# Optimization experiments

Measured on AMD Instinct MI355X. Metric: run time of the kernel, lower is better.

The kernel has to match this reference:

```python
import jax, jax.numpy as jnp
import numpy as np

N_NODES = 100000
N_EDGES = 400000
N_GRAPHS = 4096
BN_EPS = 1e-5


def _glorot(key, shape):
    fan_in, fan_out = shape
    lim = np.sqrt(6.0 / (fan_in + fan_out))
    return jax.random.uniform(key, shape, jnp.float32, -lim, lim)


def setup_inputs() -> dict:
    key = jax.random.key(0)
    ks = jax.random.split(key, 16)
    x = jax.random.normal(ks[0], (N_NODES, 373), jnp.float32)
    edge_index = jax.random.randint(ks[1], (2, N_EDGES), 0, N_NODES, jnp.int64)
    batch = jnp.sort(jax.random.randint(ks[2], (N_NODES,), 0, N_GRAPHS, jnp.int64))
    params = {
        # GIN layer 1 MLP: 373->256->256
        'W1a': _glorot(ks[3], (373, 256)), 'b1a': jnp.zeros((256,), jnp.float32),
        'W1b': _glorot(ks[4], (256, 256)), 'b1b': jnp.zeros((256,), jnp.float32),
        'g1': jnp.ones((256,), jnp.float32), 'be1': jnp.zeros((256,), jnp.float32),
        # GIN layer 2 MLP: 256->128->128
        'W2a': _glorot(ks[5], (256, 128)), 'b2a': jnp.zeros((128,), jnp.float32),
        'W2b': _glorot(ks[6], (128, 128)), 'b2b': jnp.zeros((128,), jnp.float32),
        'g2': jnp.ones((128,), jnp.float32), 'be2': jnp.zeros((128,), jnp.float32),
        # GIN layer 3 MLP: 128->64->64
        'W3a': _glorot(ks[7], (128, 64)), 'b3a': jnp.zeros((64,), jnp.float32),
        'W3b': _glorot(ks[8], (64, 64)), 'b3b': jnp.zeros((64,), jnp.float32),
        'g3': jnp.ones((64,), jnp.float32), 'be3': jnp.zeros((64,), jnp.float32),
        # head
        'Wf1': _glorot(ks[9], (64, 16)), 'bf1': jnp.zeros((16,), jnp.float32),
        'Wf2': _glorot(ks[10], (16, 1)), 'bf2': jnp.zeros((1,), jnp.float32),
    }
    return {'x': x, 'edge_index': edge_index, 'batch': batch, **params}


def _gin_conv(x, src, dst, Wa, ba, Wb, bb):
    # sum-aggregate neighbor messages (eps = 0 default in GINConv)
    agg = jax.ops.segment_sum(x[src], dst, num_segments=N_NODES)
    h = x + agg
    h = jax.nn.relu(h @ Wa + ba) @ Wb + bb
    return h


def _batchnorm(x, gamma, beta):
    mu = jnp.mean(x, axis=0)
    var = jnp.var(x, axis=0)
    return (x - mu) * jax.lax.rsqrt(var + BN_EPS) * gamma + beta


def reference(x, edge_index, batch,
              W1a, b1a, W1b, b1b, g1, be1,
              W2a, b2a, W2b, b2b, g2, be2,
              W3a, b3a, W3b, b3b, g3, be3,
              Wf1, bf1, Wf2, bf2):
    src, dst = edge_index[0], edge_index[1]
    h = jax.nn.relu(_gin_conv(x, src, dst, W1a, b1a, W1b, b1b))
    h = _batchnorm(h, g1, be1)
    h = jax.nn.relu(_gin_conv(h, src, dst, W2a, b2a, W2b, b2b))
    h = _batchnorm(h, g2, be2)
    h = jax.nn.relu(_gin_conv(h, src, dst, W3a, b3a, W3b, b3b))
    h = _batchnorm(h, g3, be3)
    # global_add_pool: [N, 64] -> [G, 64]
    pooled = jax.ops.segment_sum(h, batch, num_segments=N_GRAPHS)
    out = jax.nn.relu(pooled @ Wf1 + bf1)
    # dropout omitted (eval mode)
    out = jax.nn.relu(out @ Wf2 + bf2)
    return out.reshape(-1)
```

## Files before the change

kernel.cpp:

```cpp
#include <hip/hip_runtime.h>

#define N_NODES 100000
#define N_EDGES 400000
#define N_GRAPHS 4096
#define BN_EPS 1e-5f
#define DEG_CAP 32

typedef unsigned short ushort_t;
typedef short short8 __attribute__((ext_vector_type(8)));
typedef unsigned short ushort4v __attribute__((ext_vector_type(4)));
typedef unsigned short ushort8v __attribute__((ext_vector_type(8)));
typedef float floatx4 __attribute__((ext_vector_type(4)));

__device__ __forceinline__ ushort_t f2b(float f) {
    union { float f; unsigned u; } v; v.f = f;
    unsigned r = v.u + 0x7fffu + ((v.u >> 16) & 1u);
    return (ushort_t)(r >> 16);
}
__device__ __forceinline__ float b2f(ushort_t b) {
    union { unsigned u; float f; } v; v.u = ((unsigned)b) << 16;
    return v.f;
}

__global__ void k_pad_x(const float* __restrict__ x, ushort_t* __restrict__ xb,
                        int* __restrict__ cursor,
                        const float* __restrict__ W1a, ushort_t* __restrict__ BT1) {
    int t = threadIdx.x;
    if (blockIdx.x >= N_NODES) {
        int b = blockIdx.x - N_NODES;
        int n = b / 3, kc = b % 3;
        int k = kc * 128 + t;
        float v = (k < 373) ? W1a[(long)k * 256 + n] : 0.f;
        BT1[(long)n * 384 + k] = f2b(v);
        return;
    }
    int n = blockIdx.x;
    const float* xr = x + (long)n * 373;
    ushort_t* o = xb + (long)n * 384;
    if (t < 93) {
        float v0 = xr[t * 4 + 0], v1 = xr[t * 4 + 1], v2 = xr[t * 4 + 2], v3 = xr[t * 4 + 3];
        ushort4v s = {f2b(v0), f2b(v1), f2b(v2), f2b(v3)};
        *(ushort4v*)(o + t * 4) = s;
    } else if (t == 93) {
        o[372] = f2b(xr[372]);
        o[373] = 0; o[374] = 0; o[375] = 0;
    } else if (t == 94 || t == 95) {
        ushort4v z = {0, 0, 0, 0};
        *(ushort4v*)(o + 376 + (t - 94) * 4) = z;
    } else if (t == 96) {
        cursor[n] = 0;
    }
}

__global__ void k_fill(const int* __restrict__ src, const int* __restrict__ dst,
                       int* __restrict__ cursor, int* __restrict__ elist) {
    int e = blockIdx.x * blockDim.x + threadIdx.x;
    if (e < N_EDGES) {
        int d = dst[e];
        int slot = atomicAdd(&cursor[d], 1);
        if (slot < DEG_CAP) elist[(long)d * DEG_CAP + slot] = src[e];
    }
}

__global__ void k_prep_scaled(const float* __restrict__ W, const float* __restrict__ scsh,
                              ushort_t* __restrict__ BT, float* __restrict__ biasE,
                              int K, int Kp, int Nn) {
    int n = blockIdx.y;
    int k = blockIdx.x * 128 + threadIdx.x;
    if (k < Kp) {
        float v = (k < K) ? W[(long)k * Nn + n] * scsh[k] : 0.f;
        BT[(long)n * Kp + k] = f2b(v);
    }
    if (blockIdx.x == 0) {
        __shared__ float red[2];
        float s = 0.f;
        for (int kk = threadIdx.x; kk < K; kk += 128) s += scsh[K + kk] * W[(long)kk * Nn + n];
#pragma unroll
        for (int off = 32; off >= 1; off >>= 1) s += __shfl_xor(s, off);
        if ((threadIdx.x & 63) == 0) red[threadIdx.x >> 6] = s;
        __syncthreads();
        if (threadIdx.x == 0) biasE[n] = red[0] + red[1];
    }
}

template<int KP, int TN, bool STATS>
__global__ __launch_bounds__(256) void k_gemm(const ushort_t* __restrict__ A,
                                              const ushort_t* __restrict__ BT,
                                              const float* __restrict__ bias,
                                              ushort_t* __restrict__ C,
                                              float* __restrict__ partials,
                                              int M, int Nn, int relu) {
    __shared__ __align__(16) ushort_t As[2][128 * 32];
    __shared__ __align__(16) ushort_t Bs[2][TN * 32];
    float* swred = (float*)As;
    const int tid = threadIdx.x;
    const int wave = tid >> 6, lane = tid & 63;
    const int ln = lane & 15, kg = lane >> 4;
    const long rowBase = (long)blockIdx.y * 128;
    const int colBase = blockIdx.x * TN;

    constexpr int RT = (TN == 128) ? 4 : 2;
    const int rowOff = (TN == 128) ? ((wave >> 1) * 64) : (wave * 32);
    const int colOff = (TN == 128) ? ((wave & 1) * 64) : 0;

    const ushort_t* aSrc[2];
#pragma unroll
    for (int i = 0; i < 2; i++) {
        long r = rowBase + i * 64 + (tid >> 2);
        if (r >= M) r = M - 1;
        aSrc[i] = A + r * KP + (tid & 3) * 8;
    }
    const ushort_t* bSrc[TN / 64];
#pragma unroll
    for (int i = 0; i < TN / 64; i++) {
        long cc = colBase + i * 64 + (tid >> 2);
        bSrc[i] = BT + cc * KP + (tid & 3) * 8;
    }

    auto stage = [&](int b, int k0) {
#pragma unroll
        for (int i = 0; i < 2; i++)
            __builtin_amdgcn_global_load_lds(
                (const __attribute__((address_space(1))) void*)(aSrc[i] + k0),
                (__attribute__((address_space(3))) void*)(As[b] + wave * 512 + i * 2048), 16, 0, 0);
#pragma unroll
        for (int i = 0; i < TN / 64; i++)
            __builtin_amdgcn_global_load_lds(
                (const __attribute__((address_space(1))) void*)(bSrc[i] + k0),
                (__attribute__((address_space(3))) void*)(Bs[b] + wave * 512 + i * 2048), 16, 0, 0);
    };

    floatx4 acc[RT][4];
#pragma unroll
    for (int i = 0; i < RT; i++)
#pragma unroll
        for (int j = 0; j < 4; j++) acc[i][j] = (floatx4){0.f, 0.f, 0.f, 0.f};

    stage(0, 0);
    int cur = 0;
    for (int k0 = 0; k0 < KP; k0 += 32) {
        __syncthreads();
        if (k0 + 32 < KP) stage(cur ^ 1, k0 + 32);

        short8 afr[RT], bfr[4];
#pragma unroll
        for (int rt = 0; rt < RT; rt++)
            afr[rt] = *(const short8*)&As[cur][(rowOff + rt * 16 + ln) * 32 + kg * 8];
#pragma unroll
        for (int tn = 0; tn < 4; tn++)
            bfr[tn] = *(const short8*)&Bs[cur][(colOff + tn * 16 + ln) * 32 + kg * 8];
#pragma unroll
        for (int rt = 0; rt < RT; rt++)
#pragma unroll
            for (int tn = 0; tn < 4; tn++)
                acc[rt][tn] = __builtin_amdgcn_mfma_f32_16x16x32_bf16(afr[rt], bfr[tn], acc[rt][tn], 0, 0, 0);
        cur ^= 1;
    }

    if constexpr (STATS) {
        __syncthreads();
        for (int i = tid; i < 4 * 2 * TN; i += 256) swred[i] = 0.f;
        __syncthreads();
    }

    float sums[4] = {0.f, 0.f, 0.f, 0.f};
    float sqs[4]  = {0.f, 0.f, 0.f, 0.f};
#pragma unroll
    for (int rt = 0; rt < RT; rt++) {
#pragma unroll
        for (int tn = 0; tn < 4; tn++) {
            int gc = colBase + colOff + tn * 16 + ln;
            float bv = bias ? bias[gc] : 0.f;
#pragma unroll
            for (int r = 0; r < 4; r++) {
                long gr = rowBase + rowOff + rt * 16 + kg * 4 + r;
                if (gr < M) {
                    float v = acc[rt][tn][r] + bv;
                    if (relu) v = fmaxf(v, 0.f);
                    ushort_t sb = f2b(v);
                    C[gr * Nn + gc] = sb;
                    if (STATS) {
                        float vb = b2f(sb);
                        sums[tn] += vb;
                        sqs[tn] += vb * vb;
                    }
                }
            }
        }
    }
    if constexpr (STATS) {
#pragma unroll
        for (int tn = 0; tn < 4; tn++) {
            float s = sums[tn], q = sqs[tn];
            s += __shfl_xor(s, 16); q += __shfl_xor(q, 16);
            s += __shfl_xor(s, 32); q += __shfl_xor(q, 32);
            if (kg == 0) {
                int c = colOff + tn * 16 + ln;
                swred[wave * 2 * TN + c] = s;
                swred[wave * 2 * TN + TN + c] = q;
            }
        }
        __syncthreads();
        const int by = blockIdx.y;
        const int gyd = gridDim.y;
        for (int c = tid; c < TN; c += 256) {
            float ssum = 0.f, ssq = 0.f;
#pragma unroll
            for (int w = 0; w < 4; w++) {
                ssum += swred[w * 2 * TN + c];
                ssq  += swred[w * 2 * TN + TN + c];
            }
            long gc = colBase + c;
            partials[gc * gyd + by] = ssum;
            partials[((long)Nn + gc) * gyd + by] = ssq;
        }
    }
}

template<int KP, int TN>
__global__ __launch_bounds__(256, 4) void k_gemm_agg(const ushort_t* __restrict__ y,
                                                  const int* __restrict__ cursor,
                                                  const int* __restrict__ elist,
                                                  const float* __restrict__ badd,
                                                  const ushort_t* __restrict__ BT,
                                                  const float* __restrict__ bias,
                                                  ushort_t* __restrict__ C,
                                                  float* __restrict__ partials,
                                                  int M, int Nn) {
    __shared__ __align__(16) ushort_t Af[128 * KP];
    __shared__ __align__(16) ushort_t Bs[TN * 32];
    float* swred = (float*)Af;
    const int tid = threadIdx.x;
    const int wave = tid >> 6, lane = tid & 63;
    const int ln = lane & 15, kg = lane >> 4;
    const long rowBase = (long)blockIdx.y * 128;
    constexpr int CPR = KP / 8;
    constexpr int TPR = CPR;
    constexpr int RPS = 256 / TPR;

    {
        const int lr = tid / TPR;
        const int ck = tid % TPR;
        const int c0 = ck * 8;
        float bd[8];
#pragma unroll
        for (int j = 0; j < 8; j++) bd[j] = badd[c0 + j];
        for (int s = 0; s < 128; s += RPS) {
            int r = s + lr;
            long gr = rowBase + r; if (gr >= M) gr = M - 1;
            int cnt = cursor[gr]; if (cnt > DEG_CAP) cnt = DEG_CAP;
            const int* el = elist + gr * DEG_CAP;
            int4 e0 = *(const int4*)el;
            int4 e1 = *(const int4*)(el + 4);
            int ids[8] = {e0.x, e0.y, e0.z, e0.w, e1.x, e1.y, e1.z, e1.w};
            ushort8v sv = *(const ushort8v*)(y + gr * KP + c0);
            ushort8v rr[8];
#pragma unroll
            for (int i = 0; i < 8; i++)
                if (i < cnt) rr[i] = *(const ushort8v*)(y + (long)ids[i] * KP + c0);
            float av[8];
#pragma unroll
            for (int j = 0; j < 8; j++) av[j] = b2f(sv[j]);
#pragma unroll
            for (int i = 0; i < 8; i++)
                if (i < cnt) {
#pragma unroll
                    for (int j = 0; j < 8; j++) av[j] += b2f(rr[i][j]);
                }
            for (int i = 8; i < cnt; i++) {
                ushort8v u = *(const ushort8v*)(y + (long)el[i] * KP + c0);
#pragma unroll
                for (int j = 0; j < 8; j++) av[j] += b2f(u[j]);
            }
            ushort8v ov;
#pragma unroll
            for (int j = 0; j < 8; j++) ov[j] = f2b(fmaxf(av[j] + bd[j], 0.f));
            int cks = ck ^ (r & (CPR - 1));
            *(ushort8v*)&Af[r * KP + cks * 8] = ov;
        }
    }

    constexpr int RT = (TN == 128) ? 4 : 2;
    const int rowOff = (TN == 128) ? ((wave >> 1) * 64) : (wave * 32);
    const int colOff = (TN == 128) ? ((wave & 1) * 64) : 0;
    const ushort_t* bSrc[TN / 64];
#pragma unroll
    for (int i = 0; i < TN / 64; i++) {
        long cc = i * 64 + (tid >> 2);
        bSrc[i] = BT + cc * KP + (tid & 3) * 8;
    }
    ushort_t* bDst = Bs + wave * 512;

    floatx4 acc[RT][4];
#pragma unroll
    for (int i = 0; i < RT; i++)
#pragma unroll
        for (int j = 0; j < 4; j++) acc[i][j] = (floatx4){0.f, 0.f, 0.f, 0.f};

    for (int k0 = 0; k0 < KP; k0 += 32) {
        __syncthreads();
#pragma unroll
        for (int i = 0; i < TN / 64; i++)
            __builtin_amdgcn_global_load_lds(
                (const __attribute__((address_space(1))) void*)(bSrc[i] + k0),
                (__attribute__((address_space(3))) void*)(bDst + i * 2048), 16, 0, 0);
        __syncthreads();

        short8 afr[RT], bfr[4];
#pragma unroll
        for (int rt = 0; rt < RT; rt++) {
            int row = rowOff + rt * 16 + ln;
            int cks = ((k0 >> 3) + kg) ^ (row & (CPR - 1));
            afr[rt] = *(const short8*)&Af[row * KP + cks * 8];
        }
#pragma unroll
        for (int tn = 0; tn < 4; tn++)
            bfr[tn] = *(const short8*)&Bs[(colOff + tn * 16 + ln) * 32 + kg * 8];
#pragma unroll
        for (int rt = 0; rt < RT; rt++)
#pragma unroll
            for (int tn = 0; tn < 4; tn++)
                acc[rt][tn] = __builtin_amdgcn_mfma_f32_16x16x32_bf16(afr[rt], bfr[tn], acc[rt][tn], 0, 0, 0);
    }

    __syncthreads();
    for (int i = tid; i < 4 * 2 * TN; i += 256) swred[i] = 0.f;
    __syncthreads();

    float sums[4] = {0.f, 0.f, 0.f, 0.f};
    float sqs[4]  = {0.f, 0.f, 0.f, 0.f};
#pragma unroll
    for (int rt = 0; rt < RT; rt++) {
#pragma unroll
        for (int tn = 0; tn < 4; tn++) {
            int gc = colOff + tn * 16 + ln;
            float bv = bias[gc];
#pragma unroll
            for (int r = 0; r < 4; r++) {
                long gr = rowBase + rowOff + rt * 16 + kg * 4 + r;
                if (gr < M) {
                    float v = fmaxf(acc[rt][tn][r] + bv, 0.f);
                    ushort_t sb = f2b(v);
                    C[gr * Nn + gc] = sb;
                    float vb = b2f(sb);
                    sums[tn] += vb;
                    sqs[tn] += vb * vb;
                }
            }
        }
    }
#pragma unroll
    for (int tn = 0; tn < 4; tn++) {
        float s = sums[tn], q = sqs[tn];
        s += __shfl_xor(s, 16); q += __shfl_xor(q, 16);
        s += __shfl_xor(s, 32); q += __shfl_xor(q, 32);
        if (kg == 0) {
            int c = colOff + tn * 16 + ln;
            swred[wave * 2 * TN + c] = s;
            swred[wave * 2 * TN + TN + c] = q;
        }
    }
    __syncthreads();
    const int by = blockIdx.y;
    const int gyd = gridDim.y;
    for (int c = tid; c < TN; c += 256) {
        float ssum = 0.f, ssq = 0.f;
#pragma unroll
        for (int w = 0; w < 4; w++) {
            ssum += swred[w * 2 * TN + c];
            ssq  += swred[w * 2 * TN + TN + c];
        }
        partials[(long)c * gyd + by] = ssum;
        partials[((long)Nn + c) * gyd + by] = ssq;
    }
}

template<int D>
__global__ void k_aggregate(const ushort_t* __restrict__ y, const int* __restrict__ cursor,
                            const int* __restrict__ elist, const float* __restrict__ badd,
                            ushort_t* __restrict__ out, int nblk,
                            const float* __restrict__ Wn, ushort_t* __restrict__ BTn,
                            int KWn, int NWn) {
    int t = threadIdx.x;
    if ((int)blockIdx.x >= nblk) {
        int b = blockIdx.x - nblk;
        BTn[(long)b * KWn + t] = f2b(Wn[(long)t * NWn + b]);
        return;
    }
    const int CG = D / 4;
    const int NPB = 256 / CG;
    int n = blockIdx.x * NPB + t / CG;
    int c = (t % CG) * 4;
    if (n >= N_NODES) return;
    int cnt = cursor[n];
    if (cnt > DEG_CAP) cnt = DEG_CAP;
    const int* el = elist + (long)n * DEG_CAP;
    int4 e0 = *(const int4*)el;
    int4 e1 = *(const int4*)(el + 4);
    int ids[8] = {e0.x, e0.y, e0.z, e0.w, e1.x, e1.y, e1.z, e1.w};
    ushort4v sv = *(const ushort4v*)(y + (long)n * D + c);
    ushort4v rr[8];
#pragma unroll
    for (int i = 0; i < 8; i++)
        if (i < cnt) rr[i] = *(const ushort4v*)(y + (long)ids[i] * D + c);
    float t0 = b2f(sv.x), t1 = b2f(sv.y), t2 = b2f(sv.z), t3 = b2f(sv.w);
#pragma unroll
    for (int i = 0; i < 8; i++)
        if (i < cnt) {
            t0 += b2f(rr[i].x); t1 += b2f(rr[i].y); t2 += b2f(rr[i].z); t3 += b2f(rr[i].w);
        }
    for (int i = 8; i < cnt; i++) {
        ushort4v u = *(const ushort4v*)(y + (long)el[i] * D + c);
        t0 += b2f(u.x); t1 += b2f(u.y); t2 += b2f(u.z); t3 += b2f(u.w);
    }
    t0 = fmaxf(t0 + badd[c + 0], 0.f);
    t1 = fmaxf(t1 + badd[c + 1], 0.f);
    t2 = fmaxf(t2 + badd[c + 2], 0.f);
    t3 = fmaxf(t3 + badd[c + 3], 0.f);
    ushort4v o = {f2b(t0), f2b(t1), f2b(t2), f2b(t3)};
    *(ushort4v*)(out + (long)n * D + c) = o;
}

__global__ void k_bn(const float* __restrict__ partials, int gy,
                     const float* __restrict__ gamma, const float* __restrict__ beta,
                     float* __restrict__ scsh, int K,
                     const float* __restrict__ Wn, ushort_t* __restrict__ BTn,
                     int KWn, int NWn) {
    int b = blockIdx.x;
    int t = threadIdx.x;
    if (b >= K) {
        int p = b - K;
        int nk = KWn >> 6;
        int n = p / nk, kc = p - n * nk;
        int k = kc * 64 + t;
        BTn[(long)n * KWn + k] = f2b(Wn[(long)k * NWn + n]);
        return;
    }
    const float* ps = partials + (long)b * gy;
    const float* pq = partials + (long)(K + b) * gy;
    float s = 0.f, q = 0.f;
    for (int i = t; i < gy; i += 64) { s += ps[i]; q += pq[i]; }
#pragma unroll
    for (int off = 32; off >= 1; off >>= 1) { s += __shfl_xor(s, off); q += __shfl_xor(q, off); }
    if (t == 0) {
        float invN = 1.0f / (float)N_NODES;
        float mu = s * invN;
        float var = fmaxf(q * invN - mu * mu, 0.f);
        float sc = rsqrtf(var + BN_EPS) * gamma[b];
        scsh[b] = sc;
        scsh[K + b] = beta[b] - mu * sc;
    }
}

__global__ void k_poolhead(const ushort_t* __restrict__ h, const int* __restrict__ batch,
                           const float* __restrict__ scsh,
                           const float* __restrict__ Wf1, const float* __restrict__ bf1,
                           const float* __restrict__ Wf2, const float* __restrict__ bf2,
                           float* __restrict__ out) {
    __shared__ float pl[64];
    __shared__ float hid[16];
    int g = blockIdx.x;
    int c = threadIdx.x;
    int lo = 0, hi = N_NODES;
    while (lo < hi) { int mid = (lo + hi) >> 1; if (batch[mid] < g) lo = mid + 1; else hi = mid; }
    int start = lo;
    hi = N_NODES;
    while (lo < hi) { int mid = (lo + hi) >> 1; if (batch[mid] < g + 1) lo = mid + 1; else hi = mid; }
    int end = lo;
    float s = 0.f;
    for (int r = start; r < end; r++) s += b2f(h[(long)r * 64 + c]);
    pl[c] = s * scsh[c] + scsh[64 + c] * (float)(end - start);
    __syncthreads();
    if (c < 16) {
        float sh = bf1[c];
        for (int j = 0; j < 64; j++) sh += pl[j] * Wf1[j * 16 + c];
        hid[c] = fmaxf(sh, 0.f);
    }
    __syncthreads();
    if (c == 0) {
        float o = bf2[0];
#pragma unroll
        for (int k = 0; k < 16; k++) o += hid[k] * Wf2[k];
        out[g] = fmaxf(o, 0.f);
    }
}

extern "C" void kernel_launch(void* const* d_in, const int* in_sizes, int n_in,
                              void* d_out, int out_size, void* d_ws, size_t ws_size,
                              hipStream_t stream) {
    const float* x    = (const float*)d_in[0];
    const int*  ei    = (const int*)d_in[1];
    const int*  batch = (const int*)d_in[2];
    const float* W1a = (const float*)d_in[3];
    const float* b1a = (const float*)d_in[4];
    const float* W1b = (const float*)d_in[5];
    const float* b1b = (const float*)d_in[6];
    const float* g1  = (const float*)d_in[7];
    const float* be1 = (const float*)d_in[8];
    const float* W2a = (const float*)d_in[9];
    const float* b2a = (const float*)d_in[10];
    const float* W2b = (const float*)d_in[11];
    const float* b2b = (const float*)d_in[12];
    const float* g2  = (const float*)d_in[13];
    const float* be2 = (const float*)d_in[14];
    const float* W3a = (const float*)d_in[15];
    const float* b3a = (const float*)d_in[16];
    const float* W3b = (const float*)d_in[17];
    const float* b3b = (const float*)d_in[18];
    const float* g3  = (const float*)d_in[19];
    const float* be3 = (const float*)d_in[20];
    const float* Wf1 = (const float*)d_in[21];
    const float* bf1 = (const float*)d_in[22];
    const float* Wf2 = (const float*)d_in[23];
    const float* bf2 = (const float*)d_in[24];

    const int N = N_NODES, E = N_EDGES;
    const int* src = ei;
    const int* dst = ei + E;
    const int gy = (N + 127) / 128;

    char* wp = (char*)d_ws;
    auto carve = [&](size_t bytes) {
        char* p = wp;
        wp += (bytes + 255) & ~(size_t)255;
        return (void*)p;
    };
    ushort_t* xb     = (ushort_t*)carve((size_t)N * 384 * 2);
    ushort_t* bufA   = (ushort_t*)carve((size_t)N * 256 * 2);
    ushort_t* bufB   = (ushort_t*)carve((size_t)N * 256 * 2);
    int*      elist  = (int*)carve((size_t)N * DEG_CAP * 4);
    int*      cursor = (int*)carve((size_t)N * 4);
    ushort_t* BT1    = (ushort_t*)carve((size_t)256 * 384 * 2);
    ushort_t* BT2    = (ushort_t*)carve((size_t)256 * 384 * 2);
    float*    scsh   = (float*)carve(512 * 4);
    float*    biasE  = (float*)carve(256 * 4);
    float*    partials = (float*)carve((size_t)2 * 256 * gy * 4);

    dim3 blk(256);

    k_pad_x<<<N + 768, 128, 0, stream>>>(x, xb, cursor, W1a, BT1);
    k_fill<<<(E + 255) / 256, blk, 0, stream>>>(src, dst, cursor, elist);

    k_gemm<384, 128, false><<<dim3(2, gy), blk, 0, stream>>>(xb, BT1, nullptr, bufA, nullptr, N, 256, 0);
    k_aggregate<256><<<25000 + 256, blk, 0, stream>>>(bufA, cursor, elist, b1a, bufB, 25000, W1b, BT2, 256, 256);
    k_gemm<256, 128, true><<<dim3(2, gy), blk, 0, stream>>>(bufB, BT2, b1b, bufA, partials, N, 256, 1);
    k_bn<<<256 + 256, 64, 0, stream>>>(partials, gy, g1, be1, scsh, 256, W2b, BT2, 128, 128);

    k_prep_scaled<<<dim3(2, 128), 128, 0, stream>>>(W2a, scsh, BT1, biasE, 256, 256, 128);
    k_gemm<256, 128, false><<<dim3(1, gy), blk, 0, stream>>>(bufA, BT1, biasE, bufB, nullptr, N, 128, 0);
    k_gemm_agg<128, 128><<<dim3(1, gy), blk, 0, stream>>>(bufB, cursor, elist, b2a, BT2, b2b, bufA, partials, N, 128);
    k_bn<<<128 + 64, 64, 0, stream>>>(partials, gy, g2, be2, scsh, 128, W3b, BT2, 64, 64);

    k_prep_scaled<<<dim3(1, 64), 128, 0, stream>>>(W3a, scsh, BT1, biasE, 128, 128, 64);
    k_gemm<128, 64, false><<<dim3(1, gy), blk, 0, stream>>>(bufA, BT1, biasE, bufB, nullptr, N, 64, 0);
    k_gemm_agg<64, 64><<<dim3(1, gy), blk, 0, stream>>>(bufB, cursor, elist, b3a, BT2, b3b, bufA, partials, N, 64);
    k_bn<<<64, 64, 0, stream>>>(partials, gy, g3, be3, scsh, 64, nullptr, nullptr, 64, 64);

    k_poolhead<<<N_GRAPHS, 64, 0, stream>>>(bufA, batch, scsh, Wf1, bf1, Wf2, bf2, (float*)d_out);
}
```

Baseline: 614.3 us.

## Fuse layers 2-3, batchnorm and pooling head into one cooperative persistent kernel

Replaces the separate GEMM, gemm_agg, batchnorm, weight-prep and pool-head launches for layers 2 and 3 with a single cooperative kernel. Its phases are separated by grid-wide syncs and it iterates over row tiles persistently. The layer-3 weight transposes are folded into the first BN launch, and the head now handles one graph per wave using shuffle-based reductions. This is meant to remove per-launch overhead and tail effects between the many small kernels. The cost is grid.sync barriers and a grid capped at 1024 blocks, which may cut parallelism in the gather-heavy phases.

```diff
diff --git a/kernel.cpp b/kernel.cpp
--- a/kernel.cpp
+++ b/kernel.cpp
@@ -1,10 +1,14 @@
 #include <hip/hip_runtime.h>
+#include <hip/hip_cooperative_groups.h>
+
+namespace cg = cooperative_groups;
 
 #define N_NODES 100000
 #define N_EDGES 400000
 #define N_GRAPHS 4096
 #define BN_EPS 1e-5f
 #define DEG_CAP 32
+#define GY 782
 
 typedef unsigned short ushort_t;
 typedef short short8 __attribute__((ext_vector_type(8)));
@@ -217,164 +221,6 @@
     }
 }
 
-template<int KP, int TN>
-__global__ __launch_bounds__(256, 4) void k_gemm_agg(const ushort_t* __restrict__ y,
-                                                  const int* __restrict__ cursor,
-                                                  const int* __restrict__ elist,
-                                                  const float* __restrict__ badd,
-                                                  const ushort_t* __restrict__ BT,
-                                                  const float* __restrict__ bias,
-                                                  ushort_t* __restrict__ C,
-                                                  float* __restrict__ partials,
-                                                  int M, int Nn) {
-    __shared__ __align__(16) ushort_t Af[128 * KP];
-    __shared__ __align__(16) ushort_t Bs[TN * 32];
-    float* swred = (float*)Af;
-    const int tid = threadIdx.x;
-    const int wave = tid >> 6, lane = tid & 63;
-    const int ln = lane & 15, kg = lane >> 4;
-    const long rowBase = (long)blockIdx.y * 128;
-    constexpr int CPR = KP / 8;
-    constexpr int TPR = CPR;
-    constexpr int RPS = 256 / TPR;
-
-    {
-        const int lr = tid / TPR;
-        const int ck = tid % TPR;
-        const int c0 = ck * 8;
-        float bd[8];
-#pragma unroll
-        for (int j = 0; j < 8; j++) bd[j] = badd[c0 + j];
-        for (int s = 0; s < 128; s += RPS) {
-            int r = s + lr;
-            long gr = rowBase + r; if (gr >= M) gr = M - 1;
-            int cnt = cursor[gr]; if (cnt > DEG_CAP) cnt = DEG_CAP;
-            const int* el = elist + gr * DEG_CAP;
-            int4 e0 = *(const int4*)el;
-            int4 e1 = *(const int4*)(el + 4);
-            int ids[8] = {e0.x, e0.y, e0.z, e0.w, e1.x, e1.y, e1.z, e1.w};
-            ushort8v sv = *(const ushort8v*)(y + gr * KP + c0);
-            ushort8v rr[8];
-#pragma unroll
-            for (int i = 0; i < 8; i++)
-                if (i < cnt) rr[i] = *(const ushort8v*)(y + (long)ids[i] * KP + c0);
-            float av[8];
-#pragma unroll
-            for (int j = 0; j < 8; j++) av[j] = b2f(sv[j]);
-#pragma unroll
-            for (int i = 0; i < 8; i++)
-                if (i < cnt) {
-#pragma unroll
-                    for (int j = 0; j < 8; j++) av[j] += b2f(rr[i][j]);
-                }
-            for (int i = 8; i < cnt; i++) {
-                ushort8v u = *(const ushort8v*)(y + (long)el[i] * KP + c0);
-#pragma unroll
-                for (int j = 0; j < 8; j++) av[j] += b2f(u[j]);
-            }
-            ushort8v ov;
-#pragma unroll
-            for (int j = 0; j < 8; j++) ov[j] = f2b(fmaxf(av[j] + bd[j], 0.f));
-            int cks = ck ^ (r & (CPR - 1));
-            *(ushort8v*)&Af[r * KP + cks * 8] = ov;
-        }
-    }
-
-    constexpr int RT = (TN == 128) ? 4 : 2;
-    const int rowOff = (TN == 128) ? ((wave >> 1) * 64) : (wave * 32);
-    const int colOff = (TN == 128) ? ((wave & 1) * 64) : 0;
-    const ushort_t* bSrc[TN / 64];
-#pragma unroll
-    for (int i = 0; i < TN / 64; i++) {
-        long cc = i * 64 + (tid >> 2);
-        bSrc[i] = BT + cc * KP + (tid & 3) * 8;
-    }
-    ushort_t* bDst = Bs + wave * 512;
-
-    floatx4 acc[RT][4];
-#pragma unroll
-    for (int i = 0; i < RT; i++)
-#pragma unroll
-        for (int j = 0; j < 4; j++) acc[i][j] = (floatx4){0.f, 0.f, 0.f, 0.f};
-
-    for (int k0 = 0; k0 < KP; k0 += 32) {
-        __syncthreads();
-#pragma unroll
-        for (int i = 0; i < TN / 64; i++)
-            __builtin_amdgcn_global_load_lds(
-                (const __attribute__((address_space(1))) void*)(bSrc[i] + k0),
-                (__attribute__((address_space(3))) void*)(bDst + i * 2048), 16, 0, 0);
-        __syncthreads();
-
-        short8 afr[RT], bfr[4];
-#pragma unroll
-        for (int rt = 0; rt < RT; rt++) {
-            int row = rowOff + rt * 16 + ln;
-            int cks = ((k0 >> 3) + kg) ^ (row & (CPR - 1));
-            afr[rt] = *(const short8*)&Af[row * KP + cks * 8];
-        }
-#pragma unroll
-        for (int tn = 0; tn < 4; tn++)
-            bfr[tn] = *(const short8*)&Bs[(colOff + tn * 16 + ln) * 32 + kg * 8];
-#pragma unroll
-        for (int rt = 0; rt < RT; rt++)
-#pragma unroll
-            for (int tn = 0; tn < 4; tn++)
-                acc[rt][tn] = __builtin_amdgcn_mfma_f32_16x16x32_bf16(afr[rt], bfr[tn], acc[rt][tn], 0, 0, 0);
-    }
-
-    __syncthreads();
-    for (int i = tid; i < 4 * 2 * TN; i += 256) swred[i] = 0.f;
-    __syncthreads();
-
-    float sums[4] = {0.f, 0.f, 0.f, 0.f};
-    float sqs[4]  = {0.f, 0.f, 0.f, 0.f};
-#pragma unroll
-    for (int rt = 0; rt < RT; rt++) {
-#pragma unroll
-        for (int tn = 0; tn < 4; tn++) {
-            int gc = colOff + tn * 16 + ln;
-            float bv = bias[gc];
-#pragma unroll
-            for (int r = 0; r < 4; r++) {
-                long gr = rowBase + rowOff + rt * 16 + kg * 4 + r;
-                if (gr < M) {
-                    float v = fmaxf(acc[rt][tn][r] + bv, 0.f);
-                    ushort_t sb = f2b(v);
-                    C[gr * Nn + gc] = sb;
-                    float vb = b2f(sb);
-                    sums[tn] += vb;
-                    sqs[tn] += vb * vb;
-                }
-            }
-        }
-    }
-#pragma unroll
-    for (int tn = 0; tn < 4; tn++) {
-        float s = sums[tn], q = sqs[tn];
-        s += __shfl_xor(s, 16); q += __shfl_xor(q, 16);
-        s += __shfl_xor(s, 32); q += __shfl_xor(q, 32);
-        if (kg == 0) {
-            int c = colOff + tn * 16 + ln;
-            swred[wave * 2 * TN + c] = s;
-            swred[wave * 2 * TN + TN + c] = q;
-        }
-    }
-    __syncthreads();
-    const int by = blockIdx.y;
-    const int gyd = gridDim.y;
-    for (int c = tid; c < TN; c += 256) {
-        float ssum = 0.f, ssq = 0.f;
-#pragma unroll
-        for (int w = 0; w < 4; w++) {
-            ssum += swred[w * 2 * TN + c];
-            ssq  += swred[w * 2 * TN + TN + c];
-        }
-        partials[(long)c * gyd + by] = ssum;
-        partials[((long)Nn + c) * gyd + by] = ssq;
-    }
-}
-
 template<int D>
 __global__ void k_aggregate(const ushort_t* __restrict__ y, const int* __restrict__ cursor,
                             const int* __restrict__ elist, const float* __restrict__ badd,
@@ -425,15 +271,26 @@
                      const float* __restrict__ gamma, const float* __restrict__ beta,
                      float* __restrict__ scsh, int K,
                      const float* __restrict__ Wn, ushort_t* __restrict__ BTn,
-                     int KWn, int NWn) {
+                     int KWn, int NWn,
+                     const float* __restrict__ Wn2, ushort_t* __restrict__ BTn2,
+                     int KWn2, int NWn2) {
     int b = blockIdx.x;
     int t = threadIdx.x;
     if (b >= K) {
         int p = b - K;
         int nk = KWn >> 6;
-        int n = p / nk, kc = p - n * nk;
-        int k = kc * 64 + t;
-        BTn[(long)n * KWn + k] = f2b(Wn[(long)k * NWn + n]);
+        int tot1 = NWn * nk;
+        if (p < tot1) {
+            int n = p / nk, kc = p - n * nk;
+            int k = kc * 64 + t;
+            BTn[(long)n * KWn + k] = f2b(Wn[(long)k * NWn + n]);
+        } else {
+            p -= tot1;
+            int nk2 = KWn2 >> 6;
+            int n = p / nk2, kc = p - n * nk2;
+            int k = kc * 64 + t;
+            BTn2[(long)n * KWn2 + k] = f2b(Wn2[(long)k * NWn2 + n]);
+        }
         return;
     }
     const float* ps = partials + (long)b * gy;
@@ -452,36 +309,352 @@
     }
 }
 
-__global__ void k_poolhead(const ushort_t* __restrict__ h, const int* __restrict__ batch,
-                           const float* __restrict__ scsh,
-                           const float* __restrict__ Wf1, const float* __restrict__ bf1,
-                           const float* __restrict__ Wf2, const float* __restrict__ bf2,
-                           float* __restrict__ out) {
-    __shared__ float pl[64];
-    __shared__ float hid[16];
-    int g = blockIdx.x;
-    int c = threadIdx.x;
-    int lo = 0, hi = N_NODES;
-    while (lo < hi) { int mid = (lo + hi) >> 1; if (batch[mid] < g) lo = mid + 1; else hi = mid; }
-    int start = lo;
-    hi = N_NODES;
-    while (lo < hi) { int mid = (lo + hi) >> 1; if (batch[mid] < g + 1) lo = mid + 1; else hi = mid; }
-    int end = lo;
-    float s = 0.f;
-    for (int r = start; r < end; r++) s += b2f(h[(long)r * 64 + c]);
-    pl[c] = s * scsh[c] + scsh[64 + c] * (float)(end - start);
+
+template<int KP, int TN>
+__device__ void gemm_tile(char* smem, const ushort_t* __restrict__ A,
+                          const ushort_t* __restrict__ BT, const float* __restrict__ bias,
+                          ushort_t* __restrict__ C, int M, int Nn, int by) {
+    ushort_t* As = (ushort_t*)smem;
+    ushort_t* Bs = (ushort_t*)(smem + 128 * 32 * 2);
+    const int tid = threadIdx.x;
+    const int wave = tid >> 6, lane = tid & 63;
+    const int ln = lane & 15, kg = lane >> 4;
+    const long rowBase = (long)by * 128;
+
+    constexpr int RT = (TN == 128) ? 4 : 2;
+    const int rowOff = (TN == 128) ? ((wave >> 1) * 64) : (wave * 32);
+    const int colOff = (TN == 128) ? ((wave & 1) * 64) : 0;
+
+    const ushort_t* aSrc[2];
+#pragma unroll
+    for (int i = 0; i < 2; i++) {
+        long r = rowBase + i * 64 + (tid >> 2);
+        if (r >= M) r = M - 1;
+        aSrc[i] = A + r * KP + (tid & 3) * 8;
+    }
+    const ushort_t* bSrc[TN / 64];
+#pragma unroll
+    for (int i = 0; i < TN / 64; i++) {
+        long cc = i * 64 + (tid >> 2);
+        bSrc[i] = BT + cc * KP + (tid & 3) * 8;
+    }
+    ushort_t* aDst = As + wave * 512;
+    ushort_t* bDst = Bs + wave * 512;
+
+    floatx4 acc[RT][4];
+#pragma unroll
+    for (int i = 0; i < RT; i++)
+#pragma unroll
+        for (int j = 0; j < 4; j++) acc[i][j] = (floatx4){0.f, 0.f, 0.f, 0.f};
+
+    for (int k0 = 0; k0 < KP; k0 += 32) {
+        __syncthreads();
+#pragma unroll
+        for (int i = 0; i < 2; i++)
+            __builtin_amdgcn_global_load_lds(
+                (const __attribute__((address_space(1))) void*)(aSrc[i] + k0),
+                (__attribute__((address_space(3))) void*)(aDst + i * 2048), 16, 0, 0);
+#pragma unroll
+        for (int i = 0; i < TN / 64; i++)
+            __builtin_amdgcn_global_load_lds(
+                (const __attribute__((address_space(1))) void*)(bSrc[i] + k0),
+                (__attribute__((address_space(3))) void*)(bDst + i * 2048), 16, 0, 0);
+        __syncthreads();
+
+        short8 afr[RT], bfr[4];
+#pragma unroll
+        for (int rt = 0; rt < RT; rt++)
+            afr[rt] = *(const short8*)&As[(rowOff + rt * 16 + ln) * 32 + kg * 8];
+#pragma unroll
+        for (int tn = 0; tn < 4; tn++)
+            bfr[tn] = *(const short8*)&Bs[(colOff + tn * 16 + ln) * 32 + kg * 8];
+#pragma unroll
+        for (int rt = 0; rt < RT; rt++)
+#pragma unroll
+            for (int tn = 0; tn < 4; tn++)
+                acc[rt][tn] = __builtin_amdgcn_mfma_f32_16x16x32_bf16(afr[rt], bfr[tn], acc[rt][tn], 0, 0, 0);
+    }
     __syncthreads();
-    if (c < 16) {
-        float sh = bf1[c];
-        for (int j = 0; j < 64; j++) sh += pl[j] * Wf1[j * 16 + c];
-        hid[c] = fmaxf(sh, 0.f);
-    }
+
+#pragma unroll
+    for (int rt = 0; rt < RT; rt++) {
+#pragma unroll
+        for (int tn = 0; tn < 4; tn++) {
+            int gc = colOff + tn * 16 + ln;
+            float bv = bias[gc];
+#pragma unroll
+            for (int r = 0; r < 4; r++) {
+                long gr = rowBase + rowOff + rt * 16 + kg * 4 + r;
+                if (gr < M) C[gr * Nn + gc] = f2b(acc[rt][tn][r] + bv);
+            }
+        }
+    }
+}
+
+template<int KP, int TN>
+__device__ void gemm_agg_tile(char* smem, const ushort_t* __restrict__ y,
+                              const int* __restrict__ cursor, const int* __restrict__ elist,
+                              const float* __restrict__ badd, const ushort_t* __restrict__ BT,
+                              const float* __restrict__ bias, ushort_t* __restrict__ C,
+                              float* __restrict__ partials, int M, int Nn, int by, int gyd) {
+    ushort_t* Af = (ushort_t*)smem;
+    ushort_t* Bs = (ushort_t*)(smem + 128 * KP * 2);
+    float* swred = (float*)smem;
+    const int tid = threadIdx.x;
+    const int wave = tid >> 6, lane = tid & 63;
+    const int ln = lane & 15, kg = lane >> 4;
+    const long rowBase = (long)by * 128;
+    constexpr int CPR = KP / 8;
+    constexpr int TPR = CPR;
+    constexpr int RPS = 256 / TPR;
+
     __syncthreads();
-    if (c == 0) {
-        float o = bf2[0];
-#pragma unroll
-        for (int k = 0; k < 16; k++) o += hid[k] * Wf2[k];
-        out[g] = fmaxf(o, 0.f);
+
+    {
+        const int lr = tid / TPR;
+        const int ck = tid % TPR;
+        const int c0 = ck * 8;
+        float bd[8];
+#pragma unroll
+        for (int j = 0; j < 8; j++) bd[j] = badd[c0 + j];
+        for (int s = 0; s < 128; s += RPS) {
+            int r = s + lr;
+            long gr = rowBase + r; if (gr >= M) gr = M - 1;
+            int cnt = cursor[gr]; if (cnt > DEG_CAP) cnt = DEG_CAP;
+            const int* el = elist + gr * DEG_CAP;
+            int4 e0 = *(const int4*)el;
+            int4 e1 = *(const int4*)(el + 4);
+            int ids[8] = {e0.x, e0.y, e0.z, e0.w, e1.x, e1.y, e1.z, e1.w};
+            ushort8v sv = *(const ushort8v*)(y + gr * KP + c0);
+            ushort8v rr[8];
+#pragma unroll
+            for (int i = 0; i < 8; i++)
+                if (i < cnt) rr[i] = *(const ushort8v*)(y + (long)ids[i] * KP + c0);
+            float av[8];
+#pragma unroll
+            for (int j = 0; j < 8; j++) av[j] = b2f(sv[j]);
+#pragma unroll
+            for (int i = 0; i < 8; i++)
+                if (i < cnt) {
+#pragma unroll
+                    for (int j = 0; j < 8; j++) av[j] += b2f(rr[i][j]);
+                }
+            for (int i = 8; i < cnt; i++) {
+                ushort8v u = *(const ushort8v*)(y + (long)el[i] * KP + c0);
+#pragma unroll
+                for (int j = 0; j < 8; j++) av[j] += b2f(u[j]);
+            }
+            ushort8v ov;
+#pragma unroll
+            for (int j = 0; j < 8; j++) ov[j] = f2b(fmaxf(av[j] + bd[j], 0.f));
+            int cks = ck ^ (r & (CPR - 1));
+            *(ushort8v*)&Af[r * KP + cks * 8] = ov;
+        }
+    }
+
+    constexpr int RT = (TN == 128) ? 4 : 2;
+    const int rowOff = (TN == 128) ? ((wave >> 1) * 64) : (wave * 32);
+    const int colOff = (TN == 128) ? ((wave & 1) * 64) : 0;
+    const ushort_t* bSrc[TN / 64];
+#pragma unroll
+    for (int i = 0; i < TN / 64; i++) {
+        long cc = i * 64 + (tid >> 2);
+        bSrc[i] = BT + cc * KP + (tid & 3) * 8;
+    }
+    ushort_t* bDst = Bs + wave * 512;
+
+    floatx4 acc[RT][4];
+#pragma unroll
+    for (int i = 0; i < RT; i++)
+#pragma unroll
+        for (int j = 0; j < 4; j++) acc[i][j] = (floatx4){0.f, 0.f, 0.f, 0.f};
+
+    for (int k0 = 0; k0 < KP; k0 += 32) {
+        __syncthreads();
+#pragma unroll
+        for (int i = 0; i < TN / 64; i++)
+            __builtin_amdgcn_global_load_lds(
+                (const __attribute__((address_space(1))) void*)(bSrc[i] + k0),
+                (__attribute__((address_space(3))) void*)(bDst + i * 2048), 16, 0, 0);
+        __syncthreads();
+
+        short8 afr[RT], bfr[4];
+#pragma unroll
+        for (int rt = 0; rt < RT; rt++) {
+            int row = rowOff + rt * 16 + ln;
+            int cks = ((k0 >> 3) + kg) ^ (row & (CPR - 1));
+            afr[rt] = *(const short8*)&Af[row * KP + cks * 8];
+        }
+#pragma unroll
+        for (int tn = 0; tn < 4; tn++)
+            bfr[tn] = *(const short8*)&Bs[(colOff + tn * 16 + ln) * 32 + kg * 8];
+#pragma unroll
+        for (int rt = 0; rt < RT; rt++)
+#pragma unroll
+            for (int tn = 0; tn < 4; tn++)
+                acc[rt][tn] = __builtin_amdgcn_mfma_f32_16x16x32_bf16(afr[rt], bfr[tn], acc[rt][tn], 0, 0, 0);
+    }
+
+    __syncthreads();
+    for (int i = tid; i < 4 * 2 * TN; i += 256) swred[i] = 0.f;
+    __syncthreads();
+
+    float sums[4] = {0.f, 0.f, 0.f, 0.f};
+    float sqs[4]  = {0.f, 0.f, 0.f, 0.f};
+#pragma unroll
+    for (int rt = 0; rt < RT; rt++) {
+#pragma unroll
+        for (int tn = 0; tn < 4; tn++) {
+            int gc = colOff + tn * 16 + ln;
+            float bv = bias[gc];
+#pragma unroll
+            for (int r = 0; r < 4; r++) {
+                long gr = rowBase + rowOff + rt * 16 + kg * 4 + r;
+                if (gr < M) {
+                    float v = fmaxf(acc[rt][tn][r] + bv, 0.f);
+                    ushort_t sb = f2b(v);
+                    C[gr * Nn + gc] = sb;
+                    float vb = b2f(sb);
+                    sums[tn] += vb;
+                    sqs[tn] += vb * vb;
+                }
+            }
+        }
+    }
+#pragma unroll
+    for (int tn = 0; tn < 4; tn++) {
+        float s = sums[tn], q = sqs[tn];
+        s += __shfl_xor(s, 16); q += __shfl_xor(q, 16);
+        s += __shfl_xor(s, 32); q += __shfl_xor(q, 32);
+        if (kg == 0) {
+            int c = colOff + tn * 16 + ln;
+            swred[wave * 2 * TN + c] = s;
+            swred[wave * 2 * TN + TN + c] = q;
+        }
+    }
+    __syncthreads();
+    for (int c = tid; c < TN; c += 256) {
+        float ssum = 0.f, ssq = 0.f;
+#pragma unroll
+        for (int w = 0; w < 4; w++) {
+            ssum += swred[w * 2 * TN + c];
+            ssq  += swred[w * 2 * TN + TN + c];
+        }
+        partials[(long)c * gyd + by] = ssum;
+        partials[((long)Nn + c) * gyd + by] = ssq;
+    }
+    __syncthreads();
+}
+
+__device__ void bn_phase(char* smem, const float* __restrict__ partials, int gy,
+                         const float* __restrict__ gamma, const float* __restrict__ beta,
+                         float* __restrict__ scsh, int K) {
+    float* red = (float*)smem;
+    int wave = threadIdx.x >> 6, lane = threadIdx.x & 63;
+    for (int b = blockIdx.x; b < K; b += gridDim.x) {
+        const float* ps = partials + (long)b * gy;
+        const float* pq = partials + (long)(K + b) * gy;
+        float s = 0.f, q = 0.f;
+        for (int i = threadIdx.x; i < gy; i += 256) { s += ps[i]; q += pq[i]; }
+#pragma unroll
+        for (int off = 32; off >= 1; off >>= 1) { s += __shfl_xor(s, off); q += __shfl_xor(q, off); }
+        if (lane == 0) { red[wave] = s; red[4 + wave] = q; }
+        __syncthreads();
+        if (threadIdx.x == 0) {
+            s = red[0] + red[1] + red[2] + red[3];
+            q = red[4] + red[5] + red[6] + red[7];
+            float invN = 1.0f / (float)N_NODES;
+            float mu = s * invN;
+            float var = fmaxf(q * invN - mu * mu, 0.f);
+            float sc = rsqrtf(var + BN_EPS) * gamma[b];
+            scsh[b] = sc;
+            scsh[K + b] = beta[b] - mu * sc;
+        }
+        __syncthreads();
+    }
+}
+
+__global__ __launch_bounds__(256, 4) void k_tail(
+    ushort_t* bufA, ushort_t* bufB, const int* cursor, const int* elist,
+    const ushort_t* BT2a, const float* biasE2a, const float* b2a,
+    const ushort_t* BT2b, const float* b2b,
+    float* partials, float* scsh,
+    const float* g2, const float* be2,
+    const float* W3a, ushort_t* BT3a, float* biasE3, const float* b3a,
+    const ushort_t* BT3b, const float* b3b,
+    const float* g3, const float* be3,
+    const int* batch, const float* Wf1, const float* bf1,
+    const float* Wf2, const float* bf2, float* outp) {
+    cg::grid_group grid = cg::this_grid();
+    __shared__ __align__(16) char smem[40960];
+
+    for (int by = blockIdx.x; by < GY; by += gridDim.x)
+        gemm_tile<256, 128>(smem, bufA, BT2a, biasE2a, bufB, N_NODES, 128, by);
+    grid.sync();
+
+    for (int by = blockIdx.x; by < GY; by += gridDim.x)
+        gemm_agg_tile<128, 128>(smem, bufB, cursor, elist, b2a, BT2b, b2b, bufA, partials, N_NODES, 128, by, GY);
+    grid.sync();
+
+    bn_phase(smem, partials, GY, g2, be2, scsh, 128);
+    grid.sync();
+
+    {
+        float* red = (float*)smem;
+        int wave = threadIdx.x >> 6, lane = threadIdx.x & 63;
+        for (int n = blockIdx.x; n < 64; n += gridDim.x) {
+            int t = threadIdx.x;
+            float p = 0.f;
+            if (t < 128) {
+                float w = W3a[(long)t * 64 + n];
+                BT3a[n * 128 + t] = f2b(w * scsh[t]);
+                p = scsh[128 + t] * w;
+            }
+#pragma unroll
+            for (int off = 32; off >= 1; off >>= 1) p += __shfl_xor(p, off);
+            if (lane == 0) red[wave] = p;
+            __syncthreads();
+            if (t == 0) biasE3[n] = red[0] + red[1] + red[2] + red[3];
+            __syncthreads();
+        }
+    }
+    grid.sync();
+
+    for (int by = blockIdx.x; by < GY; by += gridDim.x)
+        gemm_tile<128, 64>(smem, bufA, BT3a, biasE3, bufB, N_NODES, 64, by);
+    grid.sync();
+
+    for (int by = blockIdx.x; by < GY; by += gridDim.x)
+        gemm_agg_tile<64, 64>(smem, bufB, cursor, elist, b3a, BT3b, b3b, bufA, partials, N_NODES, 64, by, GY);
+    grid.sync();
+
+    bn_phase(smem, partials, GY, g3, be3, scsh + 256, 64);
+    grid.sync();
+
+    {
+        const float* sc3 = scsh + 256;
+        int wave = threadIdx.x >> 6, lane = threadIdx.x & 63;
+        for (int g = blockIdx.x * 4 + wave; g < N_GRAPHS; g += gridDim.x * 4) {
+            int lo = 0, hi = N_NODES;
+            while (lo < hi) { int mid = (lo + hi) >> 1; if (batch[mid] < g) lo = mid + 1; else hi = mid; }
+            int start = lo;
+            hi = N_NODES;
+            while (lo < hi) { int mid = (lo + hi) >> 1; if (batch[mid] < g + 1) lo = mid + 1; else hi = mid; }
+            int end = lo;
+            float pl = 0.f;
+            for (int r = start; r < end; r++) pl += b2f(bufA[(long)r * 64 + lane]);
+            pl = pl * sc3[lane] + sc3[64 + lane] * (float)(end - start);
+            float hid = 0.f;
+            for (int j = 0; j < 64; j++) {
+                float v = __shfl(pl, j);
+                if (lane < 16) hid += v * Wf1[j * 16 + lane];
+            }
+            float p = 0.f;
+            if (lane < 16) p = fmaxf(hid + bf1[lane], 0.f) * Wf2[lane];
+            p += __shfl_xor(p, 8); p += __shfl_xor(p, 4);
+            p += __shfl_xor(p, 2); p += __shfl_xor(p, 1);
+            if (lane == 0) outp[g] = fmaxf(p + bf2[0], 0.f);
+        }
     }
 }
 
@@ -517,7 +690,7 @@
     const int N = N_NODES, E = N_EDGES;
     const int* src = ei;
     const int* dst = ei + E;
-    const int gy = (N + 127) / 128;
+    const int gy = GY;
 
     char* wp = (char*)d_ws;
     auto carve = [&](size_t bytes) {
@@ -532,9 +705,13 @@
     int*      cursor = (int*)carve((size_t)N * 4);
     ushort_t* BT1    = (ushort_t*)carve((size_t)256 * 384 * 2);
     ushort_t* BT2    = (ushort_t*)carve((size_t)256 * 384 * 2);
+    ushort_t* BT3a   = (ushort_t*)carve((size_t)64 * 128 * 2);
+    ushort_t* BT3b   = (ushort_t*)carve((size_t)64 * 64 * 2);
     float*    scsh   = (float*)carve(512 * 4);
     float*    biasE  = (float*)carve(256 * 4);
+    float*    biasE3 = (float*)carve(64 * 4);
     float*    partials = (float*)carve((size_t)2 * 256 * gy * 4);
+    float*    outp   = (float*)d_out;
 
     dim3 blk(256);
 
@@ -544,17 +721,24 @@
     k_gemm<384, 128, false><<<dim3(2, gy), blk, 0, stream>>>(xb, BT1, nullptr, bufA, nullptr, N, 256, 0);
     k_aggregate<256><<<25000 + 256, blk, 0, stream>>>(bufA, cursor, elist, b1a, bufB, 25000, W1b, BT2, 256, 256);
     k_gemm<256, 128, true><<<dim3(2, gy), blk, 0, stream>>>(bufB, BT2, b1b, bufA, partials, N, 256, 1);
-    k_bn<<<256 + 256, 64, 0, stream>>>(partials, gy, g1, be1, scsh, 256, W2b, BT2, 128, 128);
-
+    k_bn<<<256 + 256 + 64, 64, 0, stream>>>(partials, gy, g1, be1, scsh, 256,
+                                            W2b, BT2, 128, 128, W3b, BT3b, 64, 64);
     k_prep_scaled<<<dim3(2, 128), 128, 0, stream>>>(W2a, scsh, BT1, biasE, 256, 256, 128);
-    k_gemm<256, 128, false><<<dim3(1, gy), blk, 0, stream>>>(bufA, BT1, biasE, bufB, nullptr, N, 128, 0);
-    k_gemm_agg<128, 128><<<dim3(1, gy), blk, 0, stream>>>(bufB, cursor, elist, b2a, BT2, b2b, bufA, partials, N, 128);
-    k_bn<<<128 + 64, 64, 0, stream>>>(partials, gy, g2, be2, scsh, 128, W3b, BT2, 64, 64);
-
-    k_prep_scaled<<<dim3(1, 64), 128, 0, stream>>>(W3a, scsh, BT1, biasE, 128, 128, 64);
-    k_gemm<128, 64, false><<<dim3(1, gy), blk, 0, stream>>>(bufA, BT1, biasE, bufB, nullptr, N, 64, 0);
-    k_gemm_agg<64, 64><<<dim3(1, gy), blk, 0, stream>>>(bufB, cursor, elist, b3a, BT2, b3b, bufA, partials, N, 64);
-    k_bn<<<64, 64, 0, stream>>>(partials, gy, g3, be3, scsh, 64, nullptr, nullptr, 64, 64);
-
-    k_poolhead<<<N_GRAPHS, 64, 0, stream>>>(bufA, batch, scsh, Wf1, bf1, Wf2, bf2, (float*)d_out);
-}
+
+    int nb = 0;
+    hipOccupancyMaxActiveBlocksPerMultiprocessor(&nb, k_tail, 256, 0);
+    if (nb < 1) nb = 1;
+    int gridc = nb * 256;
+    if (gridc > 1024) gridc = 1024;
+    void* args[] = { &bufA, &bufB, &cursor, &elist,
+                     &BT1, &biasE, &b2a,
+                     &BT2, &b2b,
+                     &partials, &scsh,
+                     &g2, &be2,
+                     &W3a, &BT3a, &biasE3, &b3a,
+                     &BT3b, &b3b,
+                     &g3, &be3,
+                     &batch, &Wf1, &bf1,
+                     &Wf2, &bf2, &outp };
+    hipLaunchCooperativeKernel(k_tail, dim3(gridc), dim3(256), args, 0, stream);
+}
```

Measured after the change: 1.169 ms. 90.3% more time.
